# Optimization experiments

Hardware: AMD Instinct MI355X
Metric: run time of the kernel (lower is better)

The kernel has to match this reference:

```python
import jax, jax.numpy as jnp
import numpy as np

B, D, Q = 64, 1024, 128
V, E, H = 50000, 300, 256   # vocab, embed_dim, prealign hidden
POS_V, POS_D = 56, 12
NER_V, NER_D = 19, 8


def setup_inputs() -> dict:
    key = jax.random.key(0)
    ks = jax.random.split(key, 10)
    word_emb = (jax.random.normal(ks[0], (V, E), jnp.float32) * 0.1).at[0].set(0.0)
    pos_emb = (jax.random.normal(ks[1], (POS_V, POS_D), jnp.float32) * 0.1).at[0].set(0.0)
    ner_emb = (jax.random.normal(ks[2], (NER_V, NER_D), jnp.float32) * 0.1).at[0].set(0.0)
    proj_w = jax.random.normal(ks[3], (E, H), jnp.float32) / np.sqrt(E)
    proj_b = jnp.zeros((H,), jnp.float32)
    return {
        "query_tok": jax.random.randint(ks[4], (B, Q), 0, V),
        "doc_tok": jax.random.randint(ks[5], (B, D), 0, V),
        "doc_pos": jax.random.randint(ks[6], (B, D), 0, POS_V),
        "doc_ner": jax.random.randint(ks[7], (B, D), 0, NER_V),
        "doc_fea": jax.random.normal(ks[8], (B, D, 4), jnp.float32),
        "word_emb": word_emb,
        "proj_w": proj_w,
        "proj_b": proj_b,
        "pos_emb": pos_emb,
        "ner_emb": ner_emb,
    }


def _embed(table, idx):
    # padding_idx=0 semantics: row 0 contributes zeros
    return table[idx] * (idx != 0)[..., None].astype(table.dtype)


def reference(query_tok, doc_tok, doc_pos, doc_ner, doc_fea,
              word_emb, proj_w, proj_b, pos_emb, ner_emb):
    doc_e = _embed(word_emb, doc_tok)      # [B,D,E]
    query_e = _embed(word_emb, query_tok)  # [B,Q,E]

    # Prealign: shared Linear+ReLU proj, then bmm -> softmax -> bmm
    d_proj = jax.nn.relu(doc_e @ proj_w + proj_b)    # [B,D,H]
    q_proj = jax.nn.relu(query_e @ proj_w + proj_b)  # [B,Q,H]
    scores = jnp.einsum('bdh,bqh->bdq', d_proj, q_proj)
    attn = jax.nn.softmax(scores, axis=-1)           # softmax over query dim
    prealign = jnp.einsum('bdq,bqe->bde', attn, query_e)  # [B,D,E]

    doc_out = jnp.concatenate(
        [doc_e, prealign, _embed(ner_emb, doc_ner), _embed(pos_emb, doc_pos), doc_fea],
        axis=-1)  # [B,D,E+E+8+12+4]
    return query_e, doc_out
```

## Files before the change

### kernel.cpp

```cpp
#include <hip/hip_runtime.h>
#include <hip/hip_bf16.h>

typedef unsigned short u16;
typedef __attribute__((ext_vector_type(8))) short bf16x8;
typedef __attribute__((ext_vector_type(4))) float f32x4;

#define MFMA16(a, b, c) __builtin_amdgcn_mfma_f32_16x16x32_bf16((a), (b), (c), 0, 0, 0)

#define NB 64
#define ND 1024
#define NQ 128
#define NE 300
#define NH 256
#define KP 320
#define QETN 304
#define EBW 304
#define DOC_W 624

static __device__ __forceinline__ u16 f2bf(float f) {
  union { __bf16 h; u16 u; } c; c.h = (__bf16)f; return c.u;
}

static __device__ __forceinline__ bf16x8 pack8(float4 f0, float4 f1) {
  union { bf16x8 v; u16 u[8]; } r;
  r.u[0] = f2bf(f0.x); r.u[1] = f2bf(f0.y); r.u[2] = f2bf(f0.z); r.u[3] = f2bf(f0.w);
  r.u[4] = f2bf(f1.x); r.u[5] = f2bf(f1.y); r.u[6] = f2bf(f1.z); r.u[7] = f2bf(f1.w);
  return r.v;
}

static __device__ __forceinline__ float bf2f(u16 u) {
  union { float f; unsigned i; } x; x.i = ((unsigned)u) << 16; return x.f;
}

static __device__ __forceinline__ void bf8_to_f32(bf16x8 v, float4& f0, float4& f1) {
  union { bf16x8 b; u16 u[8]; } x; x.b = v;
  f0.x = bf2f(x.u[0]); f0.y = bf2f(x.u[1]); f0.z = bf2f(x.u[2]); f0.w = bf2f(x.u[3]);
  f1.x = bf2f(x.u[4]); f1.y = bf2f(x.u[5]); f1.z = bf2f(x.u[6]); f1.w = bf2f(x.u[7]);
}

__global__ void k_pre(const float* __restrict__ w, u16* __restrict__ wt,
                      const int* __restrict__ qtok, const float* __restrict__ emb,
                      float* __restrict__ q_out, u16* __restrict__ qet,
                      const int* __restrict__ ner, const int* __restrict__ pos,
                      const float* __restrict__ fea,
                      const float* __restrict__ ner_emb, const float* __restrict__ pos_emb,
                      float* __restrict__ doc_out,
                      const float* __restrict__ bias, u16* __restrict__ qP,
                      u16* __restrict__ embB) {
  __shared__ u16 T[64][322];
  int bx = blockIdx.x, tid = threadIdx.x;
  if (bx < 80) {
    int idx = bx * 1024 + tid;
    int n = idx / KP, k = idx % KP;
    wt[idx] = (k < NE) ? f2bf(w[k * NH + n]) : (u16)0;
  } else if (bx < 680) {
    int idx = (bx - 80) * 1024 + tid;
    int row = idx / 75, j = (idx % 75) * 4;
    float4 v = {0.f, 0.f, 0.f, 0.f};
    int t = qtok[row];
    if (t != 0) v = *(const float4*)(emb + (long)t * NE + j);
    *(float4*)(q_out + (long)row * NE + j) = v;
  } else if (bx < 1064) {
    int idx = (bx - 680) * 1024 + tid;
    int row = idx / 6, c0 = (idx % 6) * 4;
    float4 v;
    float* vp = (float*)&v;
#pragma unroll
    for (int u = 0; u < 4; ++u) {
      int c = c0 + u;
      float x;
      if (c < 8)       { int t = ner[row]; x = t ? ner_emb[t * 8 + c] : 0.f; }
      else if (c < 20) { int t = pos[row]; x = t ? pos_emb[t * 12 + (c - 8)] : 0.f; }
      else             { x = fea[(long)row * 4 + (c - 20)]; }
      vp[u] = x;
    }
    *(float4*)(doc_out + (long)row * DOC_W + 600 + c0) = v;
  } else if (bx < 1192) {
    int bxx = bx - 1064;
    int b = bxx >> 1, k0 = (bxx & 1) * 64;
    for (int i = tid; i < 64 * 75; i += 1024) {
      int row = i / 75, j = (i % 75) * 4;
      int t = qtok[b * NQ + k0 + row];
      float4 f = {0.f, 0.f, 0.f, 0.f};
      if (t != 0) f = *(const float4*)(emb + (long)t * NE + j);
      T[row][j]     = f2bf(f.x); T[row][j + 1] = f2bf(f.y);
      T[row][j + 2] = f2bf(f.z); T[row][j + 3] = f2bf(f.w);
    }
    __syncthreads();
    u16* dst = qet + (long)b * QETN * NQ + k0;
    for (int i = tid; i < QETN * 16; i += 1024) {
      int n = i / 16, kq = (i % 16) * 4;
      u16 v[4] = {0, 0, 0, 0};
      if (n < NE) {
        v[0] = T[kq][n]; v[1] = T[kq + 1][n]; v[2] = T[kq + 2][n]; v[3] = T[kq + 3][n];
      }
      *(uint2*)(dst + (long)n * NQ + kq) = *(const uint2*)v;
    }
  } else if (bx < 1320) {
    int bx2 = bx - 1192;
    int rowg = bx2 >> 2, colg = bx2 & 3;
    int ncol0 = colg * 64;
    for (int i = tid; i < 300 * 64; i += 1024) {
      int n = i & 63, k = i >> 6;
      T[n][k] = f2bf(w[k * NH + ncol0 + n]);
    }
    for (int i = tid; i < 64 * 22; i += 1024)
      T[i / 22][300 + (i % 22)] = 0;
    __syncthreads();
    int l = tid & 63, wv = tid >> 6;
    int lr = l & 15, lg = l >> 4, c0 = 8 * lg;
    int bm0 = rowg * 256 + wv * 16;
    const float* ar = emb + (long)qtok[bm0 + lr] * NE;
    f32x4 acc[4] = {};
#pragma unroll 3
    for (int ks = 0; ks < 288; ks += 32) {
      bf16x8 a0 = pack8(*(const float4*)(ar + ks + c0), *(const float4*)(ar + ks + c0 + 4));
#pragma unroll
      for (int nt = 0; nt < 4; ++nt) {
        bf16x8 bb = *(const bf16x8*)&T[nt * 16 + lr][ks + c0];
        acc[nt] = MFMA16(a0, bb, acc[nt]);
      }
    }
    {
      const int ks = 288;
      int col = ks + c0;
      float4 z = {0.f, 0.f, 0.f, 0.f};
      float4 f0 = (col + 4 <= NE) ? *(const float4*)(ar + col) : z;
      float4 f1 = (col + 8 <= NE) ? *(const float4*)(ar + col + 4) : z;
      bf16x8 a0 = pack8(f0, f1);
#pragma unroll
      for (int nt = 0; nt < 4; ++nt) {
        bf16x8 bb = *(const bf16x8*)&T[nt * 16 + lr][ks + c0];
        acc[nt] = MFMA16(a0, bb, acc[nt]);
      }
    }
#pragma unroll
    for (int nt = 0; nt < 4; ++nt) {
      int col = ncol0 + nt * 16 + lr;
      float bv = bias[col];
#pragma unroll
      for (int r = 0; r < 4; ++r) {
        int row = bm0 + 4 * lg + r;
        float v = acc[nt][r] + bv;
        v = v > 0.f ? v : 0.f;
        qP[(long)row * NH + col] = f2bf(v);
      }
    }
  } else {
    int idx = (bx - 1320) * 1024 + tid;
    if (idx < 50000 * 76) {
      int v = idx / 76, j = (idx % 76) * 4;
      u16 o[4] = {0, 0, 0, 0};
      if (j < NE) {
        float4 f = *(const float4*)(emb + (long)v * NE + j);
        o[0] = f2bf(f.x); o[1] = f2bf(f.y); o[2] = f2bf(f.z); o[3] = f2bf(f.w);
      }
      *(uint2*)(embB + (long)v * EBW + j) = *(const uint2*)o;
    }
  }
}

__launch_bounds__(256, 2)
__global__ void k_fused(const int* __restrict__ dtok, const u16* __restrict__ embB,
                        float* doc_out, const u16* __restrict__ Wt,
                        const float* __restrict__ bias,
                        const u16* __restrict__ qP, const u16* __restrict__ qeT) {
  __shared__ __align__(16) u16 dp[128][264];
  u16 (*p_lds)[136] = (u16 (*)[136]) & dp[0][0];
  int bid = blockIdx.x;
  int xcd = bid & 7, j = bid >> 3;
  int b = xcd * 8 + (j >> 3);
  int chunk = j & 7;
  int l = threadIdx.x & 63, w = threadIdx.x >> 6;
  int lr = l & 15, lg = l >> 4;
  long blkrow = (long)b * ND + chunk * 128;
  int c0 = 8 * lg;

  {
    int mrow0 = (w & 1) * 64;
    int ncol0 = (w >> 1) * 128;
    bool wr = (w >> 1) == 0;
    const u16* arow[4];
    float* drow[4];
#pragma unroll
    for (int mt = 0; mt < 4; ++mt) {
      long r = blkrow + mrow0 + mt * 16 + lr;
      arow[mt] = embB + (long)dtok[r] * EBW;
      drow[mt] = doc_out + r * DOC_W;
    }
    const u16* wp = Wt + (long)(ncol0 + lr) * KP + c0;
    f32x4 acc[4][8] = {};
#pragma unroll
    for (int it = 0; it < 5; ++it) {
      int ks0 = it * 64, ks1 = ks0 + 32;
      bf16x8 A0[4], A1[4];
#pragma unroll
      for (int mt = 0; mt < 4; ++mt) {
        A0[mt] = *(const bf16x8*)(arow[mt] + ks0 + c0);
        A1[mt] = *(const bf16x8*)(arow[mt] + ks1 + c0);
      }
      if (wr) {
#pragma unroll
        for (int mt = 0; mt < 4; ++mt) {
          float4 f0, f1;
          bf8_to_f32(A0[mt], f0, f1);
          *(float4*)(drow[mt] + ks0 + c0) = f0;
          *(float4*)(drow[mt] + ks0 + c0 + 4) = f1;
          float4 g0, g1;
          bf8_to_f32(A1[mt], g0, g1);
          int col1 = ks1 + c0;
          if (col1 + 4 <= NE) *(float4*)(drow[mt] + col1) = g0;
          if (col1 + 8 <= NE) *(float4*)(drow[mt] + col1 + 4) = g1;
        }
      }
#pragma unroll
      for (int nt = 0; nt < 8; ++nt) {
        bf16x8 b0 = *(const bf16x8*)(wp + nt * 16 * KP + ks0);
        bf16x8 b1 = *(const bf16x8*)(wp + nt * 16 * KP + ks1);
#pragma unroll
        for (int mt = 0; mt < 4; ++mt) {
          acc[mt][nt] = MFMA16(A0[mt], b0, acc[mt][nt]);
          acc[mt][nt] = MFMA16(A1[mt], b1, acc[mt][nt]);
        }
      }
    }
#pragma unroll
    for (int nt = 0; nt < 8; ++nt) {
      int col = ncol0 + nt * 16 + lr;
      float bv = bias[col];
#pragma unroll
      for (int mt = 0; mt < 4; ++mt)
#pragma unroll
        for (int r = 0; r < 4; ++r) {
          float v = acc[mt][nt][r] + bv;
          dp[mrow0 + mt * 16 + 4 * lg + r][col] = f2bf(v > 0.f ? v : 0.f);
        }
    }
  }
  __syncthreads();

  f32x4 s[2][8] = {};
  {
    const u16* qpp = qP + ((long)b * NQ + lr) * NH + 8 * lg;
#pragma unroll
    for (int ks = 0; ks < NH; ks += 32) {
      bf16x8 a0 = *(const bf16x8*)&dp[w * 32 + lr][ks + 8 * lg];
      bf16x8 a1 = *(const bf16x8*)&dp[w * 32 + 16 + lr][ks + 8 * lg];
#pragma unroll
      for (int nt = 0; nt < 8; ++nt) {
        bf16x8 bb = *(const bf16x8*)(qpp + (long)nt * 16 * NH + ks);
        s[0][nt] = MFMA16(a0, bb, s[0][nt]);
        s[1][nt] = MFMA16(a1, bb, s[1][nt]);
      }
    }
  }
  __syncthreads();

#pragma unroll
  for (int mt = 0; mt < 2; ++mt) {
    f32x4 mx;
#pragma unroll
    for (int r = 0; r < 4; ++r) {
      float m = s[mt][0][r];
#pragma unroll
      for (int nt = 1; nt < 8; ++nt) m = fmaxf(m, s[mt][nt][r]);
      mx[r] = m;
    }
#pragma unroll
    for (int d = 1; d < 16; d <<= 1)
#pragma unroll
      for (int r = 0; r < 4; ++r) mx[r] = fmaxf(mx[r], __shfl_xor(mx[r], d));
    f32x4 sum = {};
#pragma unroll
    for (int nt = 0; nt < 8; ++nt)
#pragma unroll
      for (int r = 0; r < 4; ++r) {
        float p = __expf(s[mt][nt][r] - mx[r]);
        s[mt][nt][r] = p;
        sum[r] += p;
      }
#pragma unroll
    for (int d = 1; d < 16; d <<= 1)
#pragma unroll
      for (int r = 0; r < 4; ++r) sum[r] += __shfl_xor(sum[r], d);
    f32x4 inv;
#pragma unroll
    for (int r = 0; r < 4; ++r) inv[r] = 1.0f / sum[r];
#pragma unroll
    for (int nt = 0; nt < 8; ++nt)
#pragma unroll
      for (int r = 0; r < 4; ++r)
        p_lds[w * 32 + mt * 16 + 4 * lg + r][nt * 16 + lr] = f2bf(s[mt][nt][r] * inv[r]);
  }

  const u16* qtp = qeT + (long)b * QETN * NQ;
  bf16x8 pa[2][4];
#pragma unroll
  for (int mt = 0; mt < 2; ++mt)
#pragma unroll
    for (int ksi = 0; ksi < 4; ++ksi)
      pa[mt][ksi] = *(const bf16x8*)&p_lds[w * 32 + mt * 16 + lr][ksi * 32 + 8 * lg];
#pragma unroll 2
  for (int nt = 0; nt < 19; ++nt) {
    f32x4 acc0 = {}, acc1 = {};
#pragma unroll
    for (int ksi = 0; ksi < 4; ++ksi) {
      bf16x8 bb = *(const bf16x8*)(qtp + (long)(nt * 16 + lr) * NQ + ksi * 32 + 8 * lg);
      acc0 = MFMA16(pa[0][ksi], bb, acc0);
      acc1 = MFMA16(pa[1][ksi], bb, acc1);
    }
    int col = nt * 16 + lr;
    if (col < NE) {
#pragma unroll
      for (int r = 0; r < 4; ++r) {
        long rl0 = blkrow + w * 32 + 4 * lg + r;
        doc_out[rl0 * DOC_W + 300 + col] = acc0[r];
        doc_out[(rl0 + 16) * DOC_W + 300 + col] = acc1[r];
      }
    }
  }
}

extern "C" void kernel_launch(void* const* d_in, const int* in_sizes, int n_in,
                              void* d_out, int out_size, void* d_ws, size_t ws_size,
                              hipStream_t stream) {
  const int *query_tok = nullptr, *doc_tok = nullptr, *doc_pos = nullptr, *doc_ner = nullptr;
  const float *doc_fea = nullptr, *word_emb = nullptr, *proj_w = nullptr,
              *proj_b = nullptr, *pos_emb = nullptr, *ner_emb = nullptr;
  int n65536 = 0;
  for (int i = 0; i < n_in; ++i) {
    switch (in_sizes[i]) {
      case 15000000: word_emb  = (const float*)d_in[i]; break;
      case 262144:   doc_fea   = (const float*)d_in[i]; break;
      case 76800:    proj_w    = (const float*)d_in[i]; break;
      case 8192:     query_tok = (const int*)d_in[i];   break;
      case 256:      proj_b    = (const float*)d_in[i]; break;
      case 672:      pos_emb   = (const float*)d_in[i]; break;
      case 152:      ner_emb   = (const float*)d_in[i]; break;
      case 65536:
        if (n65536 == 0)      doc_tok = (const int*)d_in[i];
        else if (n65536 == 1) doc_pos = (const int*)d_in[i];
        else                  doc_ner = (const int*)d_in[i];
        ++n65536; break;
      default: break;
    }
  }

  float* out = (float*)d_out;
  float* q_out   = out;
  float* doc_out = out + (size_t)NB * NQ * NE;

  char* ws = (char*)d_ws;
  u16* Wt   = (u16*)ws; ws += (size_t)NH * KP * 2;
  u16* qP   = (u16*)ws; ws += (size_t)NB * NQ * NH * 2;
  u16* qeT  = (u16*)ws; ws += (size_t)NB * QETN * NQ * 2;
  u16* embB = (u16*)ws; ws += ((size_t)50000 * EBW + 64) * 2;

  k_pre<<<dim3(5031), dim3(1024), 0, stream>>>(
      proj_w, Wt, query_tok, word_emb, q_out, qeT,
      doc_ner, doc_pos, doc_fea, ner_emb, pos_emb, doc_out, proj_b, qP, embB);
  k_fused<<<dim3(512), dim3(256), 0, stream>>>(
      doc_tok, embB, doc_out, Wt, proj_b, qP, qeT);
}
```

Measured before the change: 113.3 us.

## Halve fused kernel row tile to 64 rows and double block count

Each block of the fused prealign kernel now handles 64 document rows instead of 128. The four waves split the projection by 64 hidden columns each, and later each wave owns 16 rows for scores, softmax and the value product. This halves per-thread accumulators and LDS size, allows four blocks per CU, and launches 1024 blocks for more parallelism and latency hiding. In exchange, Wt and the per-batch qP/qeT operands are reloaded twice as often per row, and each wave issues fewer MFMAs per load, lowering reuse.

```diff
diff --git a/kernel.cpp b/kernel.cpp
--- a/kernel.cpp
+++ b/kernel.cpp
@@ -160,36 +160,35 @@
   }
 }
 
-__launch_bounds__(256, 2)
+__launch_bounds__(256, 4)
 __global__ void k_fused(const int* __restrict__ dtok, const u16* __restrict__ embB,
                         float* doc_out, const u16* __restrict__ Wt,
                         const float* __restrict__ bias,
                         const u16* __restrict__ qP, const u16* __restrict__ qeT) {
-  __shared__ __align__(16) u16 dp[128][264];
+  __shared__ __align__(16) u16 dp[64][264];
   u16 (*p_lds)[136] = (u16 (*)[136]) & dp[0][0];
   int bid = blockIdx.x;
   int xcd = bid & 7, j = bid >> 3;
-  int b = xcd * 8 + (j >> 3);
-  int chunk = j & 7;
+  int b = xcd * 8 + (j >> 4);
+  int chunk = j & 15;
   int l = threadIdx.x & 63, w = threadIdx.x >> 6;
   int lr = l & 15, lg = l >> 4;
-  long blkrow = (long)b * ND + chunk * 128;
+  long blkrow = (long)b * ND + chunk * 64;
   int c0 = 8 * lg;
 
   {
-    int mrow0 = (w & 1) * 64;
-    int ncol0 = (w >> 1) * 128;
-    bool wr = (w >> 1) == 0;
+    int ncol0 = w * 64;
+    bool wr = (w == 0);
     const u16* arow[4];
     float* drow[4];
 #pragma unroll
     for (int mt = 0; mt < 4; ++mt) {
-      long r = blkrow + mrow0 + mt * 16 + lr;
+      long r = blkrow + mt * 16 + lr;
       arow[mt] = embB + (long)dtok[r] * EBW;
       drow[mt] = doc_out + r * DOC_W;
     }
     const u16* wp = Wt + (long)(ncol0 + lr) * KP + c0;
-    f32x4 acc[4][8] = {};
+    f32x4 acc[4][4] = {};
 #pragma unroll
     for (int it = 0; it < 5; ++it) {
       int ks0 = it * 64, ks1 = ks0 + 32;
@@ -214,7 +213,7 @@
         }
       }
 #pragma unroll
-      for (int nt = 0; nt < 8; ++nt) {
+      for (int nt = 0; nt < 4; ++nt) {
         bf16x8 b0 = *(const bf16x8*)(wp + nt * 16 * KP + ks0);
         bf16x8 b1 = *(const bf16x8*)(wp + nt * 16 * KP + ks1);
 #pragma unroll
@@ -225,7 +224,7 @@
       }
     }
 #pragma unroll
-    for (int nt = 0; nt < 8; ++nt) {
+    for (int nt = 0; nt < 4; ++nt) {
       int col = ncol0 + nt * 16 + lr;
       float bv = bias[col];
 #pragma unroll
@@ -233,37 +232,34 @@
 #pragma unroll
         for (int r = 0; r < 4; ++r) {
           float v = acc[mt][nt][r] + bv;
-          dp[mrow0 + mt * 16 + 4 * lg + r][col] = f2bf(v > 0.f ? v : 0.f);
+          dp[mt * 16 + 4 * lg + r][col] = f2bf(v > 0.f ? v : 0.f);
         }
     }
   }
   __syncthreads();
 
-  f32x4 s[2][8] = {};
+  f32x4 s[8] = {};
   {
     const u16* qpp = qP + ((long)b * NQ + lr) * NH + 8 * lg;
 #pragma unroll
     for (int ks = 0; ks < NH; ks += 32) {
-      bf16x8 a0 = *(const bf16x8*)&dp[w * 32 + lr][ks + 8 * lg];
-      bf16x8 a1 = *(const bf16x8*)&dp[w * 32 + 16 + lr][ks + 8 * lg];
+      bf16x8 a0 = *(const bf16x8*)&dp[w * 16 + lr][ks + 8 * lg];
 #pragma unroll
       for (int nt = 0; nt < 8; ++nt) {
         bf16x8 bb = *(const bf16x8*)(qpp + (long)nt * 16 * NH + ks);
-        s[0][nt] = MFMA16(a0, bb, s[0][nt]);
-        s[1][nt] = MFMA16(a1, bb, s[1][nt]);
+        s[nt] = MFMA16(a0, bb, s[nt]);
       }
     }
   }
   __syncthreads();
 
-#pragma unroll
-  for (int mt = 0; mt < 2; ++mt) {
+  {
     f32x4 mx;
 #pragma unroll
     for (int r = 0; r < 4; ++r) {
-      float m = s[mt][0][r];
-#pragma unroll
-      for (int nt = 1; nt < 8; ++nt) m = fmaxf(m, s[mt][nt][r]);
+      float m = s[0][r];
+#pragma unroll
+      for (int nt = 1; nt < 8; ++nt) m = fmaxf(m, s[nt][r]);
       mx[r] = m;
     }
 #pragma unroll
@@ -275,8 +271,8 @@
     for (int nt = 0; nt < 8; ++nt)
 #pragma unroll
       for (int r = 0; r < 4; ++r) {
-        float p = __expf(s[mt][nt][r] - mx[r]);
-        s[mt][nt][r] = p;
+        float p = __expf(s[nt][r] - mx[r]);
+        s[nt][r] = p;
         sum[r] += p;
       }
 #pragma unroll
@@ -290,33 +286,27 @@
     for (int nt = 0; nt < 8; ++nt)
 #pragma unroll
       for (int r = 0; r < 4; ++r)
-        p_lds[w * 32 + mt * 16 + 4 * lg + r][nt * 16 + lr] = f2bf(s[mt][nt][r] * inv[r]);
+        p_lds[w * 16 + 4 * lg + r][nt * 16 + lr] = f2bf(s[nt][r] * inv[r]);
   }
 
   const u16* qtp = qeT + (long)b * QETN * NQ;
-  bf16x8 pa[2][4];
-#pragma unroll
-  for (int mt = 0; mt < 2; ++mt)
-#pragma unroll
-    for (int ksi = 0; ksi < 4; ++ksi)
-      pa[mt][ksi] = *(const bf16x8*)&p_lds[w * 32 + mt * 16 + lr][ksi * 32 + 8 * lg];
+  bf16x8 pa[4];
+#pragma unroll
+  for (int ksi = 0; ksi < 4; ++ksi)
+    pa[ksi] = *(const bf16x8*)&p_lds[w * 16 + lr][ksi * 32 + c0];
 #pragma unroll 2
   for (int nt = 0; nt < 19; ++nt) {
-    f32x4 acc0 = {}, acc1 = {};
+    f32x4 acc0 = {};
 #pragma unroll
     for (int ksi = 0; ksi < 4; ++ksi) {
-      bf16x8 bb = *(const bf16x8*)(qtp + (long)(nt * 16 + lr) * NQ + ksi * 32 + 8 * lg);
-      acc0 = MFMA16(pa[0][ksi], bb, acc0);
-      acc1 = MFMA16(pa[1][ksi], bb, acc1);
+      bf16x8 bb = *(const bf16x8*)(qtp + (long)(nt * 16 + lr) * NQ + ksi * 32 + c0);
+      acc0 = MFMA16(pa[ksi], bb, acc0);
     }
     int col = nt * 16 + lr;
     if (col < NE) {
 #pragma unroll
-      for (int r = 0; r < 4; ++r) {
-        long rl0 = blkrow + w * 32 + 4 * lg + r;
-        doc_out[rl0 * DOC_W + 300 + col] = acc0[r];
-        doc_out[(rl0 + 16) * DOC_W + 300 + col] = acc1[r];
-      }
+      for (int r = 0; r < 4; ++r)
+        doc_out[(blkrow + w * 16 + 4 * lg + r) * DOC_W + 300 + col] = acc0[r];
     }
   }
 }
@@ -359,6 +349,6 @@
   k_pre<<<dim3(5031), dim3(1024), 0, stream>>>(
       proj_w, Wt, query_tok, word_emb, q_out, qeT,
       doc_ner, doc_pos, doc_fea, ner_emb, pos_emb, doc_out, proj_b, qP, embB);
-  k_fused<<<dim3(512), dim3(256), 0, stream>>>(
+  k_fused<<<dim3(1024), dim3(256), 0, stream>>>(
       doc_tok, embB, doc_out, Wt, proj_b, qP, qeT);
 }
```

After: 165.1 us. 1.46x slower.

## Give each wave full-width 32-row projection tile and drop block barrier

Applied to the files above, without the earlier changes.

The doc projection GEMM tile split changes from 64 rows by 128 columns per wave to 32 rows by all 256 columns per wave. Each wave now produces exactly the rows it consumes in the following score GEMM, so the __syncthreads between projection and scores is removed. Every wave now also writes its own doc_emb rows, instead of only half the waves doing all the writes. The cost is doubled B-matrix (weight) fragment loads per A fragment, and accumulator register use stays at 32 f32x4 tiles per wave.

```diff
diff --git a/kernel.cpp b/kernel.cpp
--- a/kernel.cpp
+++ b/kernel.cpp
@@ -177,67 +177,61 @@
   int c0 = 8 * lg;
 
   {
-    int mrow0 = (w & 1) * 64;
-    int ncol0 = (w >> 1) * 128;
-    bool wr = (w >> 1) == 0;
-    const u16* arow[4];
-    float* drow[4];
-#pragma unroll
-    for (int mt = 0; mt < 4; ++mt) {
-      long r = blkrow + mrow0 + mt * 16 + lr;
-      arow[mt] = embB + (long)dtok[r] * EBW;
-      drow[mt] = doc_out + r * DOC_W;
-    }
-    const u16* wp = Wt + (long)(ncol0 + lr) * KP + c0;
-    f32x4 acc[4][8] = {};
-#pragma unroll
-    for (int it = 0; it < 5; ++it) {
-      int ks0 = it * 64, ks1 = ks0 + 32;
-      bf16x8 A0[4], A1[4];
-#pragma unroll
-      for (int mt = 0; mt < 4; ++mt) {
-        A0[mt] = *(const bf16x8*)(arow[mt] + ks0 + c0);
-        A1[mt] = *(const bf16x8*)(arow[mt] + ks1 + c0);
-      }
-      if (wr) {
-#pragma unroll
-        for (int mt = 0; mt < 4; ++mt) {
-          float4 f0, f1;
-          bf8_to_f32(A0[mt], f0, f1);
-          *(float4*)(drow[mt] + ks0 + c0) = f0;
-          *(float4*)(drow[mt] + ks0 + c0 + 4) = f1;
-          float4 g0, g1;
-          bf8_to_f32(A1[mt], g0, g1);
-          int col1 = ks1 + c0;
-          if (col1 + 4 <= NE) *(float4*)(drow[mt] + col1) = g0;
-          if (col1 + 8 <= NE) *(float4*)(drow[mt] + col1 + 4) = g1;
+    long r0 = blkrow + w * 32 + lr;
+    long r1 = r0 + 16;
+    const u16* arow0 = embB + (long)dtok[r0] * EBW;
+    const u16* arow1 = embB + (long)dtok[r1] * EBW;
+    float* drow0 = doc_out + r0 * DOC_W;
+    float* drow1 = doc_out + r1 * DOC_W;
+    const u16* wp = Wt + (long)lr * KP + c0;
+    f32x4 acc[2][16] = {};
+#pragma unroll
+    for (int half = 0; half < 2; ++half) {
+      int base = half * 160;
+      bf16x8 A0[5], A1[5];
+#pragma unroll
+      for (int ss = 0; ss < 5; ++ss) {
+        A0[ss] = *(const bf16x8*)(arow0 + base + ss * 32 + c0);
+        A1[ss] = *(const bf16x8*)(arow1 + base + ss * 32 + c0);
+      }
+#pragma unroll
+      for (int ss = 0; ss < 5; ++ss) {
+        int col = base + ss * 32 + c0;
+        float4 f0, f1, g0, g1;
+        bf8_to_f32(A0[ss], f0, f1);
+        bf8_to_f32(A1[ss], g0, g1);
+        if (col + 8 <= NE) {
+          *(float4*)(drow0 + col) = f0; *(float4*)(drow0 + col + 4) = f1;
+          *(float4*)(drow1 + col) = g0; *(float4*)(drow1 + col + 4) = g1;
+        } else {
+          if (col + 4 <= NE) { *(float4*)(drow0 + col) = f0; *(float4*)(drow1 + col) = g0; }
+          if (col + 8 <= NE) { *(float4*)(drow0 + col + 4) = f1; *(float4*)(drow1 + col + 4) = g1; }
         }
       }
 #pragma unroll
-      for (int nt = 0; nt < 8; ++nt) {
-        bf16x8 b0 = *(const bf16x8*)(wp + nt * 16 * KP + ks0);
-        bf16x8 b1 = *(const bf16x8*)(wp + nt * 16 * KP + ks1);
-#pragma unroll
-        for (int mt = 0; mt < 4; ++mt) {
-          acc[mt][nt] = MFMA16(A0[mt], b0, acc[mt][nt]);
-          acc[mt][nt] = MFMA16(A1[mt], b1, acc[mt][nt]);
+      for (int ss = 0; ss < 5; ++ss) {
+        int ks = base + ss * 32;
+#pragma unroll
+        for (int nt = 0; nt < 16; ++nt) {
+          bf16x8 bb = *(const bf16x8*)(wp + nt * 16 * KP + ks);
+          acc[0][nt] = MFMA16(A0[ss], bb, acc[0][nt]);
+          acc[1][nt] = MFMA16(A1[ss], bb, acc[1][nt]);
         }
       }
     }
 #pragma unroll
-    for (int nt = 0; nt < 8; ++nt) {
-      int col = ncol0 + nt * 16 + lr;
+    for (int nt = 0; nt < 16; ++nt) {
+      int col = nt * 16 + lr;
       float bv = bias[col];
 #pragma unroll
-      for (int mt = 0; mt < 4; ++mt)
-#pragma unroll
-        for (int r = 0; r < 4; ++r) {
-          float v = acc[mt][nt][r] + bv;
-          dp[mrow0 + mt * 16 + 4 * lg + r][col] = f2bf(v > 0.f ? v : 0.f);
-        }
-    }
-  }
-  __syncthreads();
+      for (int r = 0; r < 4; ++r) {
+        float v0 = acc[0][nt][r] + bv;
+        float v1 = acc[1][nt][r] + bv;
+        dp[w * 32 + 4 * lg + r][col] = f2bf(v0 > 0.f ? v0 : 0.f);
+        dp[w * 32 + 16 + 4 * lg + r][col] = f2bf(v1 > 0.f ? v1 : 0.f);
+      }
+    }
+  }
 
   f32x4 s[2][8] = {};
   {
```

Measured after the change: 147.1 us. 1.3x slower.
